# Performance work log

Hardware: AMD Instinct MI355X
Metric: run time of the kernel (lower is better)

The kernel has to match this reference:

```python
import jax, jax.numpy as jnp
import numpy as np

B, N, D, H = 4, 2048, 256, 4
DH = D // H          # 64
SCALE = DH ** (-0.5)
LN_EPS = 1e-5


def setup_inputs() -> dict:
    key = jax.random.key(0)
    ks = jax.random.split(key, 16)
    g = lambda k, shape, fan_in: jax.random.normal(k, shape, jnp.float32) / np.sqrt(fan_in)
    # Weights stored as [in, out] (pre-transposed vs torch Linear)
    return {
        "x0": jax.random.normal(ks[0], (B, N, D), jnp.float32),
        "x1": jax.random.normal(ks[1], (B, N, D), jnp.float32),
        "Wqk": g(ks[2], (D, D), D), "bqk": jnp.zeros((D,), jnp.float32),
        "Wv": g(ks[3], (D, D), D), "bv": jnp.zeros((D,), jnp.float32),
        "Wout": g(ks[4], (D, D), D), "bout": jnp.zeros((D,), jnp.float32),
        "Wf1": g(ks[5], (2 * D, 2 * D), 2 * D), "bf1": jnp.zeros((2 * D,), jnp.float32),
        "ln_g": jnp.ones((2 * D,), jnp.float32), "ln_b": jnp.zeros((2 * D,), jnp.float32),
        "Wf2": g(ks[6], (2 * D, D), 2 * D), "bf2": jnp.zeros((D,), jnp.float32),
    }


def _split_heads(t):
    # [B,N,D] -> [B,H,N,DH]
    b, n, _ = t.shape
    return t.reshape(b, n, H, DH).transpose(0, 2, 1, 3)


def _merge_heads(t):
    # [B,H,N,DH] -> [B,N,D]
    b, h, n, dh = t.shape
    return t.transpose(0, 2, 1, 3).reshape(b, n, h * dh)


def _layernorm(x, g, b):
    mu = jnp.mean(x, axis=-1, keepdims=True)
    var = jnp.mean(jnp.square(x - mu), axis=-1, keepdims=True)
    return (x - mu) * jax.lax.rsqrt(var + LN_EPS) * g + b


def reference(x0, x1, Wqk, bqk, Wv, bv, Wout, bout, Wf1, bf1, ln_g, ln_b, Wf2, bf2):
    qk0 = _split_heads(x0 @ Wqk + bqk)   # [B,H,N,DH]
    qk1 = _split_heads(x1 @ Wqk + bqk)
    v0 = _split_heads(x0 @ Wv + bv)
    v1 = _split_heads(x1 @ Wv + bv)

    ss = SCALE ** 0.5
    sim = jnp.einsum('bhid,bhjd->bhij', qk0 * ss, qk1 * ss)  # shared score matrix
    attn01 = jax.nn.softmax(sim, axis=-1)   # normalize over j
    attn10 = jax.nn.softmax(sim, axis=-2)   # normalize over i (== softmax(sim^T) transposed)
    m0 = jnp.einsum('bhij,bhjd->bhid', attn01, v1)
    m1 = jnp.einsum('bhji,bhjd->bhid', attn10, v0)

    m0 = _merge_heads(m0) @ Wout + bout   # [B,N,D]
    m1 = _merge_heads(m1) @ Wout + bout

    def ffn(x):
        h = x @ Wf1 + bf1                 # [B,N,2D]
        h = jax.nn.gelu(_layernorm(h, ln_g, ln_b), approximate=False)
        return h @ Wf2 + bf2              # [B,N,D]

    y0 = x0 + ffn(jnp.concatenate([x0, m0], axis=-1))
    y1 = x1 + ffn(jnp.concatenate([x1, m1], axis=-1))
    return (y0, y1)
```

## Files before the change

kernel.cpp:

```cpp
#include <hip/hip_runtime.h>
#include <hip/hip_bf16.h>
#include <math.h>

typedef __bf16 bf16;
typedef __attribute__((ext_vector_type(8))) __bf16 bf16x8;
typedef __attribute__((ext_vector_type(4))) __bf16 bf16x4;
typedef __attribute__((ext_vector_type(2))) __bf16 bf16x2;
typedef __attribute__((ext_vector_type(4))) float f32x4;
typedef __attribute__((ext_vector_type(16))) float f32x16;
typedef __attribute__((ext_vector_type(4))) unsigned u32x4;

#define MFMA(a,b,c)   __builtin_amdgcn_mfma_f32_16x16x32_bf16(a,b,c,0,0,0)
#define MFMA32(a,b,c) __builtin_amdgcn_mfma_f32_32x32x16_bf16(a,b,c,0,0,0)

static constexpr int Bb = 4, Nn = 2048, Hh = 4;
static constexpr int Mrows = Bb * Nn;
static constexpr float SS2 = 0.4246609001440095f;

__device__ __forceinline__ void lds16(const bf16* src, bf16* dst) {
  __builtin_amdgcn_global_load_lds(
      (const __attribute__((address_space(1))) void*)src,
      (__attribute__((address_space(3))) void*)dst, 16, 0, 0);
}

__device__ __forceinline__ f32x16 zero16() {
  f32x16 t;
#pragma unroll
  for (int i = 0; i < 16; ++i) t[i] = 0.f;
  return t;
}

__global__ __launch_bounds__(256) void prep_k(
    const float* Wqk, const float* Wv, const float* Wout,
    const float* Wf1, const float* Wf2, const float* x0, const float* x1,
    bf16* wqkv_t, bf16* wout_t, bf16* wf1_t, bf16* wf2_t,
    bf16* xb0, bf16* xb1) {
  int id = blockIdx.x * 256 + threadIdx.x;
  if (id < 65536) { int k = id >> 8, n = id & 255; wqkv_t[n*256 + k] = (bf16)Wqk[id]; return; }
  id -= 65536;
  if (id < 65536) { int k = id >> 8, n = id & 255; wqkv_t[(256 + n)*256 + k] = (bf16)Wv[id]; return; }
  id -= 65536;
  if (id < 65536) { int k = id >> 8, n = id & 255; wout_t[n*256 + k] = (bf16)Wout[id]; return; }
  id -= 65536;
  if (id < 262144) { int k = id >> 9, n = id & 511; wf1_t[n*512 + k] = (bf16)Wf1[id]; return; }
  id -= 262144;
  if (id < 131072) { int k = id >> 8, n = id & 255; wf2_t[n*512 + k] = (bf16)Wf2[id]; return; }
  id -= 131072;
  if (id < 1048576) {
    const float* xs = (id < 524288) ? x0 : x1;
    bf16* xd = (id < 524288) ? xb0 : xb1;
    int j = (id < 524288) ? id : id - 524288;
    f32x4 v = *reinterpret_cast<const f32x4*>(&xs[(size_t)j * 4]);
    bf16x4 o; o[0] = (bf16)v[0]; o[1] = (bf16)v[1]; o[2] = (bf16)v[2]; o[3] = (bf16)v[3];
    *reinterpret_cast<bf16x4*>(&xd[(size_t)j * 4]) = o;
  }
}

template<int MODE>
__global__ __launch_bounds__(256, 3) void gemm_k(
    const bf16* Aa0, const bf16* Aa1, const bf16* Ac0, const bf16* Ac1,
    const bf16* Wt, const float* bias,
    bf16* ob0, bf16* ob1, float* of0, float* of1,
    const float* res0, const float* res1) {
  constexpr int KD  = (MODE == 3 || MODE == 4) ? 512 : 256;
  constexpr int LDA = (MODE == 4) ? 512 : 256;
  constexpr int NKC = KD / 64;

  const int z = blockIdx.z;
  const bf16* Aa = z ? Aa1 : Aa0;
  const bf16* Ac = z ? Ac1 : Ac0;
  bf16*  ob = z ? ob1 : ob0;
  float* of = z ? of1 : of0;
  const float* res = z ? res1 : res0;

  const int tid = threadIdx.x;
  const int lane = tid & 63;
  const int w = tid >> 6;
  const int wr = w >> 1, wc = w & 1;
  const int m0r = blockIdx.x * 128;
  const int n0 = blockIdx.y * 64;
  const int r15 = lane & 15, g = lane >> 4, rb = r15 & 7;
  const int l3 = lane >> 3, l7 = lane & 7;
  const int swzc = (l7 ^ l3) * 8;

  __shared__ bf16 At[2][8192];
  __shared__ bf16 Bt[2][4096];

  const bf16* aA = Aa + (size_t)(m0r + w*32 + l3) * LDA + swzc;
  const bf16* aC = (MODE == 3) ? (Ac + (size_t)(m0r + w*32 + l3) * 256 + swzc) : nullptr;
  const bf16* bB = Wt + (size_t)(n0 + w*16 + l3) * KD + swzc;
  const int adst = (w*32) * 64;
  const int bdst = (w*16) * 64;

  auto stage = [&](int buf, int kc) {
    const bf16* ab; int kcol;
    if constexpr (MODE == 3) {
      if (kc < 4) { ab = aA; kcol = kc * 64; } else { ab = aC; kcol = (kc - 4) * 64; }
    } else { ab = aA; kcol = kc * 64; }
#pragma unroll
    for (int i = 0; i < 4; i++)
      lds16(ab + kcol + (size_t)i * 8 * LDA, &At[buf][adst + i*512]);
#pragma unroll
    for (int i = 0; i < 2; i++)
      lds16(bB + kc*64 + (size_t)i * 8 * KD, &Bt[buf][bdst + i*512]);
  };

  f32x4 acc[4][2];
#pragma unroll
  for (int i = 0; i < 4; i++)
#pragma unroll
    for (int j = 0; j < 2; j++) acc[i][j] = f32x4{0.f, 0.f, 0.f, 0.f};

  const int rx0 = ((0*4 + g) ^ rb) << 4;
  const int rx1 = ((1*4 + g) ^ rb) << 4;

  auto compute = [&](int cur) {
    const char* Ap = (const char*)&At[cur][0];
    const char* Bp = (const char*)&Bt[cur][0];
    __builtin_amdgcn_s_setprio(1);
#pragma unroll
    for (int ks = 0; ks < 2; ++ks) {
      const int rx = ks ? rx1 : rx0;
      bf16x8 af[4], bfr[2];
#pragma unroll
      for (int mf = 0; mf < 4; ++mf)
        af[mf] = *reinterpret_cast<const bf16x8*>(Ap + (wr*64 + mf*16 + r15) * 128 + rx);
#pragma unroll
      for (int nf = 0; nf < 2; ++nf)
        bfr[nf] = *reinterpret_cast<const bf16x8*>(Bp + (wc*32 + nf*16 + r15) * 128 + rx);
#pragma unroll
      for (int mf = 0; mf < 4; ++mf)
#pragma unroll
        for (int nf = 0; nf < 2; ++nf)
          acc[mf][nf] = MFMA(af[mf], bfr[nf], acc[mf][nf]);
    }
    __builtin_amdgcn_s_setprio(0);
  };

  stage(0, 0);
  int cur = 0;
  for (int kc = 0; kc < NKC - 1; ++kc) {
    stage(cur ^ 1, kc + 1);
    asm volatile("s_waitcnt vmcnt(6)" ::: "memory");
    __builtin_amdgcn_sched_barrier(0);
    __builtin_amdgcn_s_barrier();
    __builtin_amdgcn_sched_barrier(0);
    compute(cur);
    asm volatile("s_waitcnt lgkmcnt(0)" ::: "memory");
    __builtin_amdgcn_sched_barrier(0);
    __builtin_amdgcn_s_barrier();
    __builtin_amdgcn_sched_barrier(0);
    cur ^= 1;
  }
  asm volatile("s_waitcnt vmcnt(0)" ::: "memory");
  __builtin_amdgcn_sched_barrier(0);
  __builtin_amdgcn_s_barrier();
  __builtin_amdgcn_sched_barrier(0);
  compute(cur);

#pragma unroll
  for (int mf = 0; mf < 4; ++mf)
#pragma unroll
    for (int nf = 0; nf < 2; ++nf) {
      f32x4 c = acc[mf][nf];
      int cg = n0 + wc*32 + nf*16 + r15;
#pragma unroll
      for (int r = 0; r < 4; ++r) {
        int rg = m0r + wr*64 + mf*16 + g*4 + r;
        if constexpr (MODE == 5) {
          int b = rg >> 11, n = rg & 2047;
          if (cg < 256) {
            float val = (c[r] + bias[cg]) * SS2;
            int h = cg >> 6, dh = cg & 63;
            ob[(((size_t)(b*Hh + h)) * Nn + n) * 64 + dh] = (bf16)val;
          } else {
            int cg2 = cg - 256;
            float val = c[r] + res[cg2];
            int h = cg2 >> 6, dh = cg2 & 63;
            ((bf16*)of)[(((size_t)(b*Hh + h)) * 64 + dh) * Nn + n] = (bf16)val;
          }
        } else {
          float val = c[r] + bias[cg];
          if constexpr (MODE == 2) {
            ob[(size_t)rg * 256 + cg] = (bf16)val;
          } else if constexpr (MODE == 3) {
            ob[(size_t)rg * 512 + cg] = (bf16)val;
          } else {
            of[(size_t)rg * 256 + cg] = val + (float)Ac[(size_t)rg * 256 + cg];
          }
        }
      }
    }
}

__global__ __launch_bounds__(256, 2) void attn_k(
    const bf16* qks0, const bf16* qks1, const bf16* vT0, const bf16* vT1,
    bf16* m0o, bf16* m1o) {
  const int B = blockIdx.x + 16 * (blockIdx.y + 16 * blockIdx.z);
  const int xcd = B & 7, kk = B >> 3;
  const int group = 4 * xcd + (kk >> 4);
  const int it = kk & 15;
  const int bh = group & 15, dir = group >> 4;

  const bf16* Q  = (dir ? qks1 : qks0) + (size_t)bh * (Nn * 64);
  const bf16* Kp = (dir ? qks0 : qks1) + (size_t)bh * (Nn * 64);
  const bf16* Vp = (dir ? vT0  : vT1 ) + (size_t)bh * (64 * Nn);
  bf16* out = dir ? m1o : m0o;
  const int b = bh >> 2, h = bh & 3;

  const int tid = threadIdx.x, lane = tid & 63, w = tid >> 6;
  const int l31 = lane & 31, hi = lane >> 5, xr = l31 & 7;
  const int iw = it * 128 + w * 32;

  __shared__ bf16 Kt[2][4096];
  __shared__ bf16 Vt[2][4096];

  bf16x8 qf[4];
#pragma unroll
  for (int kt = 0; kt < 4; ++kt)
    qf[kt] = *reinterpret_cast<const bf16x8*>(
        &Q[(size_t)(iw + l31) * 64 + kt*16 + hi*8]);

  bf16x8 ones;
#pragma unroll
  for (int i = 0; i < 8; ++i) ones[i] = (bf16)1.0f;

  f32x16 acc[2]; acc[0] = zero16(); acc[1] = zero16();
  f32x16 rsacc = zero16();

  const int l3 = lane >> 3, l7 = lane & 7;
  const int swz = ((l7 ^ l3) * 8);
  const bf16* ks0 = Kp + (size_t)(w*16 +     l3) * 64 + swz;
  const bf16* ks1 = Kp + (size_t)(w*16 + 8 + l3) * 64 + swz;
  const bf16* vs0 = Vp + (size_t)(w*16 +     l3) * 2048 + swz;
  const bf16* vs1 = Vp + (size_t)(w*16 + 8 + l3) * 2048 + swz;
  const int kd0 = (w*16    ) * 64;
  const int kd1 = (w*16 + 8) * 64;

  auto stage = [&](int buf, int j0) {
    lds16(ks0 + (size_t)j0 * 64, &Kt[buf][kd0]);
    lds16(ks1 + (size_t)j0 * 64, &Kt[buf][kd1]);
    lds16(vs0 + j0,              &Vt[buf][kd0]);
    lds16(vs1 + j0,              &Vt[buf][kd1]);
  };

  int kby[2][4], vby[2][4];
#pragma unroll
  for (int jm = 0; jm < 2; ++jm)
#pragma unroll
    for (int kt = 0; kt < 4; ++kt)
      kby[jm][kt] = (jm*32 + l31) * 128 + (((2*kt + hi) ^ xr) << 4);
#pragma unroll
  for (int nt = 0; nt < 2; ++nt)
#pragma unroll
    for (int gg = 0; gg < 4; ++gg)
      vby[nt][gg] = (nt*32 + l31) * 128 + (((2*gg + hi) ^ xr) << 4);

  auto compute_tile = [&](int cur) {
    const char* Kb = (const char*)&Kt[cur][0];
    const char* Vb = (const char*)&Vt[cur][0];
    f32x16 st[2];
    __builtin_amdgcn_s_setprio(1);
#pragma unroll
    for (int jm = 0; jm < 2; ++jm) {
      f32x16 t = zero16();
#pragma unroll
      for (int kt = 0; kt < 4; ++kt) {
        bf16x8 kf = *reinterpret_cast<const bf16x8*>(Kb + kby[jm][kt]);
        t = MFMA32(kf, qf[kt], t);
      }
      st[jm] = t;
    }
    __builtin_amdgcn_s_setprio(0);
    bf16x8 pa[4];
#pragma unroll
    for (int jm = 0; jm < 2; ++jm) {
      unsigned dw[8];
#pragma unroll
      for (int s = 0; s < 8; ++s) {
        float e0 = __builtin_amdgcn_exp2f(st[jm][2*s]);
        float e1 = __builtin_amdgcn_exp2f(st[jm][2*s + 1]);
        bf16x2 p; p[0] = (bf16)e0; p[1] = (bf16)e1;
        dw[s] = __builtin_bit_cast(unsigned, p);
      }
#pragma unroll
      for (int kt2 = 0; kt2 < 2; ++kt2) {
        unsigned a0 = dw[4*kt2 + 0], b0 = dw[4*kt2 + 2];
        unsigned a1 = dw[4*kt2 + 1], b1 = dw[4*kt2 + 3];
        asm volatile("v_permlane32_swap_b32 %0, %1" : "+v"(a0), "+v"(b0));
        asm volatile("v_permlane32_swap_b32 %0, %1" : "+v"(a1), "+v"(b1));
        u32x4 uu; uu[0] = a0; uu[1] = a1; uu[2] = b0; uu[3] = b1;
        pa[jm*2 + kt2] = __builtin_bit_cast(bf16x8, uu);
      }
    }
    __builtin_amdgcn_s_setprio(1);
#pragma unroll
    for (int gg = 0; gg < 4; ++gg) {
      rsacc = MFMA32(pa[gg], ones, rsacc);
#pragma unroll
      for (int nt = 0; nt < 2; ++nt) {
        bf16x8 vf = *reinterpret_cast<const bf16x8*>(Vb + vby[nt][gg]);
        acc[nt] = MFMA32(pa[gg], vf, acc[nt]);
      }
    }
    __builtin_amdgcn_s_setprio(0);
  };

  stage(0, 0);
  int cur = 0;
  for (int jt = 0; jt < 31; ++jt) {
    stage(cur ^ 1, (jt + 1) << 6);
    asm volatile("s_waitcnt vmcnt(4)" ::: "memory");
    __builtin_amdgcn_sched_barrier(0);
    __builtin_amdgcn_s_barrier();
    __builtin_amdgcn_sched_barrier(0);
    compute_tile(cur);
    asm volatile("s_waitcnt lgkmcnt(0)" ::: "memory");
    __builtin_amdgcn_sched_barrier(0);
    __builtin_amdgcn_s_barrier();
    __builtin_amdgcn_sched_barrier(0);
    cur ^= 1;
  }
  asm volatile("s_waitcnt vmcnt(0)" ::: "memory");
  __builtin_amdgcn_sched_barrier(0);
  __builtin_amdgcn_s_barrier();
  __builtin_amdgcn_sched_barrier(0);
  compute_tile(cur);

#pragma unroll
  for (int r = 0; r < 16; ++r) {
    float inv = 1.0f / rsacc[r];
    int row = iw + (r & 3) + 8*(r >> 2) + 4*hi;
#pragma unroll
    for (int nt = 0; nt < 2; ++nt) {
      int col = h*64 + nt*32 + l31;
      out[((size_t)b * Nn + row) * 256 + col] = (bf16)(acc[nt][r] * inv);
    }
  }
}

__global__ __launch_bounds__(256) void ln_gelu_k(
    bf16* hg, const float* g, const float* bb) {
  const size_t row = blockIdx.x;
  const int tid = threadIdx.x;
  bf16* hr = hg + row * 512;
  bf16x2 v2 = *reinterpret_cast<const bf16x2*>(&hr[tid * 2]);
  float vx = (float)v2[0], vy = (float)v2[1];
  float s = vx + vy;
  float sq = vx * vx + vy * vy;
#pragma unroll
  for (int m = 1; m < 64; m <<= 1) {
    s += __shfl_xor(s, m);
    sq += __shfl_xor(sq, m);
  }
  __shared__ float ws_s[4], ws_q[4];
  int w = tid >> 6, lane = tid & 63;
  if (lane == 0) { ws_s[w] = s; ws_q[w] = sq; }
  __syncthreads();
  s = ws_s[0] + ws_s[1] + ws_s[2] + ws_s[3];
  sq = ws_q[0] + ws_q[1] + ws_q[2] + ws_q[3];
  float mu = s * (1.f / 512.f);
  float var = sq * (1.f / 512.f) - mu * mu;
  float rsv = rsqrtf(var + 1e-5f);
  bf16x2 o2;
#pragma unroll
  for (int i = 0; i < 2; i++) {
    int c = tid * 2 + i;
    float xv = i ? vy : vx;
    float xn = (xv - mu) * rsv * g[c] + bb[c];
    float ge = 0.5f * xn * (1.f + erff(xn * 0.70710678118f));
    o2[i] = (bf16)ge;
  }
  *reinterpret_cast<bf16x2*>(&hr[tid * 2]) = o2;
}

extern "C" void kernel_launch(void* const* d_in, const int* in_sizes, int n_in,
                              void* d_out, int out_size, void* d_ws, size_t ws_size,
                              hipStream_t stream) {
  (void)in_sizes; (void)n_in; (void)out_size; (void)ws_size;
  const float* x0   = (const float*)d_in[0];
  const float* x1   = (const float*)d_in[1];
  const float* Wqk  = (const float*)d_in[2];
  const float* bqk  = (const float*)d_in[3];
  const float* Wv   = (const float*)d_in[4];
  const float* bv   = (const float*)d_in[5];
  const float* Wout = (const float*)d_in[6];
  const float* bout = (const float*)d_in[7];
  const float* Wf1  = (const float*)d_in[8];
  const float* bf1  = (const float*)d_in[9];
  const float* ln_g = (const float*)d_in[10];
  const float* ln_b = (const float*)d_in[11];
  const float* Wf2  = (const float*)d_in[12];
  const float* bf2  = (const float*)d_in[13];
  float* y = (float*)d_out;

  bf16* p = (bf16*)d_ws;
  bf16* wqkv_t = p; p += 131072;
  bf16* wout_t = p; p += 65536;
  bf16* wf1_t  = p; p += 262144;
  bf16* wf2_t  = p; p += 131072;
  bf16* xb0  = p; p += 2097152;
  bf16* xb1  = p; p += 2097152;
  bf16* qks0 = p; p += 2097152;
  bf16* qks1 = p; p += 2097152;
  bf16* vT0  = p; p += 2097152;
  bf16* vT1  = p; p += 2097152;
  bf16* m0   = p; p += 2097152;
  bf16* m1   = p; p += 2097152;
  bf16* mo0  = p; p += 2097152;
  bf16* mo1  = p; p += 2097152;
  bf16* hg0  = p; p += 4194304;
  bf16* hg1  = p; p += 4194304;

  dim3 blk(256);
  prep_k<<<6400, blk, 0, stream>>>(Wqk, Wv, Wout, Wf1, Wf2, x0, x1,
                                   wqkv_t, wout_t, wf1_t, wf2_t, xb0, xb1);
  gemm_k<5><<<dim3(64, 8, 2), blk, 0, stream>>>(xb0, xb1, nullptr, nullptr, wqkv_t, bqk,
                                                qks0, qks1, (float*)vT0, (float*)vT1, bv, bv);
  attn_k<<<dim3(16, 16, 2), blk, 0, stream>>>(qks0, qks1, vT0, vT1, m0, m1);
  gemm_k<2><<<dim3(64, 4, 2), blk, 0, stream>>>(m0, m1, nullptr, nullptr, wout_t, bout,
                                                mo0, mo1, nullptr, nullptr, nullptr, nullptr);
  gemm_k<3><<<dim3(64, 8, 2), blk, 0, stream>>>(xb0, xb1, mo0, mo1, wf1_t, bf1,
                                                hg0, hg1, nullptr, nullptr, nullptr, nullptr);
  ln_gelu_k<<<dim3(16384), blk, 0, stream>>>(hg0, ln_g, ln_b);
  gemm_k<4><<<dim3(64, 4, 2), blk, 0, stream>>>(hg0, hg1, xb0, xb1, wf2_t, bf2,
                                                nullptr, nullptr, y, y + 2097152, nullptr, nullptr);
}
```

Before: 129.7 us.

## Fold Wout into Wf1, widen GEMM tiles, deepen attention pipeline, vectorize LN

Precomputes Wout·Wf1[256:] and a folded bias with a small GEMM, so the separate output-projection GEMM and its intermediate buffer go away. The QKV and FFN1 GEMMs move to 128-wide N tiles. Attention switches to a 4-stage K/V ring with one barrier per tile and accumulates row sums in scalars instead of an MFMA against a ones vector. LayerNorm+GELU now processes one row per wavefront with 8-wide vector loads and no LDS reduction. The weight fold adds an extra bf16 rounding step and a small launch, and the larger tiles lower the allowed occupancy.

```diff
diff --git a/kernel.cpp b/kernel.cpp
--- a/kernel.cpp
+++ b/kernel.cpp
@@ -14,7 +14,6 @@
 #define MFMA32(a,b,c) __builtin_amdgcn_mfma_f32_32x32x16_bf16(a,b,c,0,0,0)
 
 static constexpr int Bb = 4, Nn = 2048, Hh = 4;
-static constexpr int Mrows = Bb * Nn;
 static constexpr float SS2 = 0.4246609001440095f;
 
 __device__ __forceinline__ void lds16(const bf16* src, bf16* dst) {
@@ -31,19 +30,25 @@
 }
 
 __global__ __launch_bounds__(256) void prep_k(
-    const float* Wqk, const float* Wv, const float* Wout,
+    const float* Wqk, const float* Wv, const float* Wout, const float* bout,
     const float* Wf1, const float* Wf2, const float* x0, const float* x1,
-    bf16* wqkv_t, bf16* wout_t, bf16* wf1_t, bf16* wf2_t,
+    bf16* wqkv_t, bf16* wout_b, bf16* wfold_t, bf16* wf1b_t, bf16* wf2_t,
     bf16* xb0, bf16* xb1) {
   int id = blockIdx.x * 256 + threadIdx.x;
   if (id < 65536) { int k = id >> 8, n = id & 255; wqkv_t[n*256 + k] = (bf16)Wqk[id]; return; }
   id -= 65536;
   if (id < 65536) { int k = id >> 8, n = id & 255; wqkv_t[(256 + n)*256 + k] = (bf16)Wv[id]; return; }
   id -= 65536;
-  if (id < 65536) { int k = id >> 8, n = id & 255; wout_t[n*256 + k] = (bf16)Wout[id]; return; }
-  id -= 65536;
-  if (id < 262144) { int k = id >> 9, n = id & 511; wf1_t[n*512 + k] = (bf16)Wf1[id]; return; }
-  id -= 262144;
+  if (id < 98304) {
+    if (id < 65536) { wout_b[id] = (bf16)Wout[id]; }
+    else { int id3 = id - 65536; int r = id3 >> 8, k = id3 & 255;
+           wout_b[(256 + r)*256 + k] = (r == 0) ? (bf16)bout[k] : (bf16)0.f; }
+    return; }
+  id -= 98304;
+  if (id < 131072) { int o = id & 511, k = id >> 9; wfold_t[o*512 + k] = (bf16)Wf1[k*512 + o]; return; }
+  id -= 131072;
+  if (id < 131072) { int o = id & 511, k = id >> 9; wf1b_t[o*256 + k] = (bf16)Wf1[(256 + k)*512 + o]; return; }
+  id -= 131072;
   if (id < 131072) { int k = id >> 8, n = id & 255; wf2_t[n*512 + k] = (bf16)Wf2[id]; return; }
   id -= 131072;
   if (id < 1048576) {
@@ -56,8 +61,8 @@
   }
 }
 
-template<int MODE>
-__global__ __launch_bounds__(256, 3) void gemm_k(
+template<int MODE, int BN, int MINW>
+__global__ __launch_bounds__(256, MINW) void gemm_k(
     const bf16* Aa0, const bf16* Aa1, const bf16* Ac0, const bf16* Ac1,
     const bf16* Wt, const float* bias,
     bf16* ob0, bf16* ob1, float* of0, float* of1,
@@ -65,6 +70,7 @@
   constexpr int KD  = (MODE == 3 || MODE == 4) ? 512 : 256;
   constexpr int LDA = (MODE == 4) ? 512 : 256;
   constexpr int NKC = KD / 64;
+  constexpr int NF  = BN / 32;
 
   const int z = blockIdx.z;
   const bf16* Aa = z ? Aa1 : Aa0;
@@ -78,19 +84,19 @@
   const int w = tid >> 6;
   const int wr = w >> 1, wc = w & 1;
   const int m0r = blockIdx.x * 128;
-  const int n0 = blockIdx.y * 64;
+  const int n0 = blockIdx.y * BN;
   const int r15 = lane & 15, g = lane >> 4, rb = r15 & 7;
   const int l3 = lane >> 3, l7 = lane & 7;
   const int swzc = (l7 ^ l3) * 8;
 
   __shared__ bf16 At[2][8192];
-  __shared__ bf16 Bt[2][4096];
+  __shared__ bf16 Bt[2][BN * 64];
 
   const bf16* aA = Aa + (size_t)(m0r + w*32 + l3) * LDA + swzc;
   const bf16* aC = (MODE == 3) ? (Ac + (size_t)(m0r + w*32 + l3) * 256 + swzc) : nullptr;
-  const bf16* bB = Wt + (size_t)(n0 + w*16 + l3) * KD + swzc;
+  const bf16* bB = Wt + (size_t)(n0 + w*(BN/4) + l3) * KD + swzc;
   const int adst = (w*32) * 64;
-  const int bdst = (w*16) * 64;
+  const int bdst = (w*(BN/4)) * 64;
 
   auto stage = [&](int buf, int kc) {
     const bf16* ab; int kcol;
@@ -101,15 +107,15 @@
     for (int i = 0; i < 4; i++)
       lds16(ab + kcol + (size_t)i * 8 * LDA, &At[buf][adst + i*512]);
 #pragma unroll
-    for (int i = 0; i < 2; i++)
+    for (int i = 0; i < NF; i++)
       lds16(bB + kc*64 + (size_t)i * 8 * KD, &Bt[buf][bdst + i*512]);
   };
 
-  f32x4 acc[4][2];
+  f32x4 acc[4][NF];
 #pragma unroll
   for (int i = 0; i < 4; i++)
 #pragma unroll
-    for (int j = 0; j < 2; j++) acc[i][j] = f32x4{0.f, 0.f, 0.f, 0.f};
+    for (int j = 0; j < NF; j++) acc[i][j] = f32x4{0.f, 0.f, 0.f, 0.f};
 
   const int rx0 = ((0*4 + g) ^ rb) << 4;
   const int rx1 = ((1*4 + g) ^ rb) << 4;
@@ -121,17 +127,17 @@
 #pragma unroll
     for (int ks = 0; ks < 2; ++ks) {
       const int rx = ks ? rx1 : rx0;
-      bf16x8 af[4], bfr[2];
+      bf16x8 af[4], bfr[NF];
 #pragma unroll
       for (int mf = 0; mf < 4; ++mf)
         af[mf] = *reinterpret_cast<const bf16x8*>(Ap + (wr*64 + mf*16 + r15) * 128 + rx);
 #pragma unroll
-      for (int nf = 0; nf < 2; ++nf)
-        bfr[nf] = *reinterpret_cast<const bf16x8*>(Bp + (wc*32 + nf*16 + r15) * 128 + rx);
+      for (int nf = 0; nf < NF; ++nf)
+        bfr[nf] = *reinterpret_cast<const bf16x8*>(Bp + (wc*(BN/2) + nf*16 + r15) * 128 + rx);
 #pragma unroll
       for (int mf = 0; mf < 4; ++mf)
 #pragma unroll
-        for (int nf = 0; nf < 2; ++nf)
+        for (int nf = 0; nf < NF; ++nf)
           acc[mf][nf] = MFMA(af[mf], bfr[nf], acc[mf][nf]);
     }
     __builtin_amdgcn_s_setprio(0);
@@ -141,7 +147,8 @@
   int cur = 0;
   for (int kc = 0; kc < NKC - 1; ++kc) {
     stage(cur ^ 1, kc + 1);
-    asm volatile("s_waitcnt vmcnt(6)" ::: "memory");
+    if constexpr (NF == 4) asm volatile("s_waitcnt vmcnt(8)" ::: "memory");
+    else                   asm volatile("s_waitcnt vmcnt(6)" ::: "memory");
     __builtin_amdgcn_sched_barrier(0);
     __builtin_amdgcn_s_barrier();
     __builtin_amdgcn_sched_barrier(0);
@@ -161,9 +168,9 @@
 #pragma unroll
   for (int mf = 0; mf < 4; ++mf)
 #pragma unroll
-    for (int nf = 0; nf < 2; ++nf) {
+    for (int nf = 0; nf < NF; ++nf) {
       f32x4 c = acc[mf][nf];
-      int cg = n0 + wc*32 + nf*16 + r15;
+      int cg = n0 + wc*(BN/2) + nf*16 + r15;
 #pragma unroll
       for (int r = 0; r < 4; ++r) {
         int rg = m0r + wr*64 + mf*16 + g*4 + r;
@@ -174,20 +181,18 @@
             int h = cg >> 6, dh = cg & 63;
             ob[(((size_t)(b*Hh + h)) * Nn + n) * 64 + dh] = (bf16)val;
           } else {
-            int cg2 = cg - 256;
-            float val = c[r] + res[cg2];
-            int h = cg2 >> 6, dh = cg2 & 63;
+            int c2 = cg - 256;
+            float val = c[r] + res[c2];
+            int h = c2 >> 6, dh = c2 & 63;
             ((bf16*)of)[(((size_t)(b*Hh + h)) * 64 + dh) * Nn + n] = (bf16)val;
           }
+        } else if constexpr (MODE == 6) {
+          if (rg < 256) ob[(size_t)cg * 512 + 256 + rg] = (bf16)c[r];
+          else if (rg == 256) of[cg] = c[r] + bias[cg];
+        } else if constexpr (MODE == 3) {
+          ob[(size_t)rg * 512 + cg] = (bf16)(c[r] + bias[cg]);
         } else {
-          float val = c[r] + bias[cg];
-          if constexpr (MODE == 2) {
-            ob[(size_t)rg * 256 + cg] = (bf16)val;
-          } else if constexpr (MODE == 3) {
-            ob[(size_t)rg * 512 + cg] = (bf16)val;
-          } else {
-            of[(size_t)rg * 256 + cg] = val + (float)Ac[(size_t)rg * 256 + cg];
-          }
+          of[(size_t)rg * 256 + cg] = c[r] + bias[cg] + (float)Ac[(size_t)rg * 256 + cg];
         }
       }
     }
@@ -212,8 +217,9 @@
   const int l31 = lane & 31, hi = lane >> 5, xr = l31 & 7;
   const int iw = it * 128 + w * 32;
 
-  __shared__ bf16 Kt[2][4096];
-  __shared__ bf16 Vt[2][4096];
+  __shared__ bf16 Kt[4][4096];
+  __shared__ bf16 Vt[4][4096];
+  __shared__ float Rt[4][32];
 
   bf16x8 qf[4];
 #pragma unroll
@@ -221,12 +227,8 @@
     qf[kt] = *reinterpret_cast<const bf16x8*>(
         &Q[(size_t)(iw + l31) * 64 + kt*16 + hi*8]);
 
-  bf16x8 ones;
-#pragma unroll
-  for (int i = 0; i < 8; ++i) ones[i] = (bf16)1.0f;
-
   f32x16 acc[2]; acc[0] = zero16(); acc[1] = zero16();
-  f32x16 rsacc = zero16();
+  float rsum = 0.f;
 
   const int l3 = lane >> 3, l7 = lane & 7;
   const int swz = ((l7 ^ l3) * 8);
@@ -280,6 +282,7 @@
       for (int s = 0; s < 8; ++s) {
         float e0 = __builtin_amdgcn_exp2f(st[jm][2*s]);
         float e1 = __builtin_amdgcn_exp2f(st[jm][2*s + 1]);
+        rsum += e0 + e1;
         bf16x2 p; p[0] = (bf16)e0; p[1] = (bf16)e1;
         dw[s] = __builtin_bit_cast(unsigned, p);
       }
@@ -296,7 +299,6 @@
     __builtin_amdgcn_s_setprio(1);
 #pragma unroll
     for (int gg = 0; gg < 4; ++gg) {
-      rsacc = MFMA32(pa[gg], ones, rsacc);
 #pragma unroll
       for (int nt = 0; nt < 2; ++nt) {
         bf16x8 vf = *reinterpret_cast<const bf16x8*>(Vb + vby[nt][gg]);
@@ -306,30 +308,35 @@
     __builtin_amdgcn_s_setprio(0);
   };
 
-  stage(0, 0);
-  int cur = 0;
-  for (int jt = 0; jt < 31; ++jt) {
-    stage(cur ^ 1, (jt + 1) << 6);
-    asm volatile("s_waitcnt vmcnt(4)" ::: "memory");
+  stage(0, 0); stage(1, 1 << 6); stage(2, 2 << 6);
+  for (int jt = 0; jt < 30; ++jt) {
+    asm volatile("s_waitcnt vmcnt(8)" ::: "memory");
     __builtin_amdgcn_sched_barrier(0);
     __builtin_amdgcn_s_barrier();
     __builtin_amdgcn_sched_barrier(0);
-    compute_tile(cur);
-    asm volatile("s_waitcnt lgkmcnt(0)" ::: "memory");
-    __builtin_amdgcn_sched_barrier(0);
-    __builtin_amdgcn_s_barrier();
-    __builtin_amdgcn_sched_barrier(0);
-    cur ^= 1;
+    stage((jt + 3) & 3, (jt + 3) << 6);
+    compute_tile(jt & 3);
   }
+  asm volatile("s_waitcnt vmcnt(4)" ::: "memory");
+  __builtin_amdgcn_sched_barrier(0);
+  __builtin_amdgcn_s_barrier();
+  __builtin_amdgcn_sched_barrier(0);
+  compute_tile(2);
   asm volatile("s_waitcnt vmcnt(0)" ::: "memory");
   __builtin_amdgcn_sched_barrier(0);
   __builtin_amdgcn_s_barrier();
   __builtin_amdgcn_sched_barrier(0);
-  compute_tile(cur);
-
+  compute_tile(3);
+
+  rsum += __shfl_xor(rsum, 32);
+  if (lane < 32) Rt[w][l31] = rsum;
+  f32x4 rv[4];
+#pragma unroll
+  for (int q = 0; q < 4; ++q)
+    rv[q] = *reinterpret_cast<const f32x4*>(&Rt[w][8*q + 4*hi]);
 #pragma unroll
   for (int r = 0; r < 16; ++r) {
-    float inv = 1.0f / rsacc[r];
+    float inv = 1.0f / rv[r >> 2][r & 3];
     int row = iw + (r & 3) + 8*(r >> 2) + 4*hi;
 #pragma unroll
     for (int nt = 0; nt < 2; ++nt) {
@@ -341,37 +348,33 @@
 
 __global__ __launch_bounds__(256) void ln_gelu_k(
     bf16* hg, const float* g, const float* bb) {
-  const size_t row = blockIdx.x;
-  const int tid = threadIdx.x;
-  bf16* hr = hg + row * 512;
-  bf16x2 v2 = *reinterpret_cast<const bf16x2*>(&hr[tid * 2]);
-  float vx = (float)v2[0], vy = (float)v2[1];
-  float s = vx + vy;
-  float sq = vx * vx + vy * vy;
-#pragma unroll
-  for (int m = 1; m < 64; m <<= 1) {
-    s += __shfl_xor(s, m);
-    sq += __shfl_xor(sq, m);
-  }
-  __shared__ float ws_s[4], ws_q[4];
-  int w = tid >> 6, lane = tid & 63;
-  if (lane == 0) { ws_s[w] = s; ws_q[w] = sq; }
-  __syncthreads();
-  s = ws_s[0] + ws_s[1] + ws_s[2] + ws_s[3];
-  sq = ws_q[0] + ws_q[1] + ws_q[2] + ws_q[3];
+  const int row = (blockIdx.x << 2) + (threadIdx.x >> 6);
+  const int lane = threadIdx.x & 63;
+  bf16* hr = hg + (size_t)row * 512 + lane * 8;
+  bf16x8 v = *reinterpret_cast<const bf16x8*>(hr);
+  float f[8];
+  float s = 0.f, sq = 0.f;
+#pragma unroll
+  for (int i = 0; i < 8; ++i) { f[i] = (float)v[i]; s += f[i]; sq += f[i]*f[i]; }
+#pragma unroll
+  for (int m = 1; m < 64; m <<= 1) { s += __shfl_xor(s, m); sq += __shfl_xor(sq, m); }
   float mu = s * (1.f / 512.f);
   float var = sq * (1.f / 512.f) - mu * mu;
   float rsv = rsqrtf(var + 1e-5f);
-  bf16x2 o2;
-#pragma unroll
-  for (int i = 0; i < 2; i++) {
-    int c = tid * 2 + i;
-    float xv = i ? vy : vx;
-    float xn = (xv - mu) * rsv * g[c] + bb[c];
+  f32x4 g0 = *reinterpret_cast<const f32x4*>(&g[lane*8]);
+  f32x4 g1 = *reinterpret_cast<const f32x4*>(&g[lane*8 + 4]);
+  f32x4 b0 = *reinterpret_cast<const f32x4*>(&bb[lane*8]);
+  f32x4 b1 = *reinterpret_cast<const f32x4*>(&bb[lane*8 + 4]);
+  bf16x8 o;
+#pragma unroll
+  for (int i = 0; i < 8; ++i) {
+    float gv = (i < 4) ? g0[i] : g1[i-4];
+    float bv = (i < 4) ? b0[i] : b1[i-4];
+    float xn = (f[i] - mu) * rsv * gv + bv;
     float ge = 0.5f * xn * (1.f + erff(xn * 0.70710678118f));
-    o2[i] = (bf16)ge;
+    o[i] = (bf16)ge;
   }
-  *reinterpret_cast<bf16x2*>(&hr[tid * 2]) = o2;
+  *reinterpret_cast<bf16x8*>(hr) = o;
 }
 
 extern "C" void kernel_launch(void* const* d_in, const int* in_sizes, int n_in,
@@ -396,9 +399,11 @@
 
   bf16* p = (bf16*)d_ws;
   bf16* wqkv_t = p; p += 131072;
-  bf16* wout_t = p; p += 65536;
-  bf16* wf1_t  = p; p += 262144;
+  bf16* wout_b = p; p += 98304;
+  bf16* wfold_t = p; p += 262144;
+  bf16* wf1b_t = p; p += 131072;
   bf16* wf2_t  = p; p += 131072;
+  float* bfold = (float*)p; p += 1024;
   bf16* xb0  = p; p += 2097152;
   bf16* xb1  = p; p += 2097152;
   bf16* qks0 = p; p += 2097152;
@@ -407,22 +412,24 @@
   bf16* vT1  = p; p += 2097152;
   bf16* m0   = p; p += 2097152;
   bf16* m1   = p; p += 2097152;
-  bf16* mo0  = p; p += 2097152;
-  bf16* mo1  = p; p += 2097152;
   bf16* hg0  = p; p += 4194304;
   bf16* hg1  = p; p += 4194304;
 
   dim3 blk(256);
-  prep_k<<<6400, blk, 0, stream>>>(Wqk, Wv, Wout, Wf1, Wf2, x0, x1,
-                                   wqkv_t, wout_t, wf1_t, wf2_t, xb0, xb1);
-  gemm_k<5><<<dim3(64, 8, 2), blk, 0, stream>>>(xb0, xb1, nullptr, nullptr, wqkv_t, bqk,
-                                                qks0, qks1, (float*)vT0, (float*)vT1, bv, bv);
+  prep_k<<<6528, blk, 0, stream>>>(Wqk, Wv, Wout, bout, Wf1, Wf2, x0, x1,
+                                   wqkv_t, wout_b, wfold_t, wf1b_t, wf2_t, xb0, xb1);
+  gemm_k<6,128,2><<<dim3(3, 4, 1), blk, 0, stream>>>(
+      wout_b, wout_b, nullptr, nullptr, wf1b_t, bf1,
+      wfold_t, wfold_t, bfold, bfold, nullptr, nullptr);
+  gemm_k<5,128,2><<<dim3(64, 4, 2), blk, 0, stream>>>(
+      xb0, xb1, nullptr, nullptr, wqkv_t, bqk,
+      qks0, qks1, (float*)vT0, (float*)vT1, bv, bv);
   attn_k<<<dim3(16, 16, 2), blk, 0, stream>>>(qks0, qks1, vT0, vT1, m0, m1);
-  gemm_k<2><<<dim3(64, 4, 2), blk, 0, stream>>>(m0, m1, nullptr, nullptr, wout_t, bout,
-                                                mo0, mo1, nullptr, nullptr, nullptr, nullptr);
-  gemm_k<3><<<dim3(64, 8, 2), blk, 0, stream>>>(xb0, xb1, mo0, mo1, wf1_t, bf1,
-                                                hg0, hg1, nullptr, nullptr, nullptr, nullptr);
-  ln_gelu_k<<<dim3(16384), blk, 0, stream>>>(hg0, ln_g, ln_b);
-  gemm_k<4><<<dim3(64, 4, 2), blk, 0, stream>>>(hg0, hg1, xb0, xb1, wf2_t, bf2,
-                                                nullptr, nullptr, y, y + 2097152, nullptr, nullptr);
-}
+  gemm_k<3,128,2><<<dim3(64, 4, 2), blk, 0, stream>>>(
+      xb0, xb1, m0, m1, wfold_t, bfold,
+      hg0, hg1, nullptr, nullptr, nullptr, nullptr);
+  ln_gelu_k<<<dim3(4096), blk, 0, stream>>>(hg0, ln_g, ln_b);
+  gemm_k<4,64,3><<<dim3(64, 4, 2), blk, 0, stream>>>(
+      hg0, hg1, xb0, xb1, wf2_t, bf2,
+      nullptr, nullptr, y, y + 2097152, nullptr, nullptr);
+}
```

Measured after the change: 130.4 us. Within noise of the previous version (+0.5%).
